# Optimization experiments

Hardware: AMD Instinct MI355X
Metric: run time of the kernel (lower is better)

The kernel has to match this reference:

```python
import jax, jax.numpy as jnp
import numpy as np

B, C, D, H, W = 8, 1, 128, 160, 128

def setup_inputs() -> dict:
    key = jax.random.key(0)
    kx, kb = jax.random.split(key)
    x = jax.random.normal(kx, (B, C, D, H, W), dtype=jnp.float32)
    base_volume = jax.random.normal(kb, (C, D, H, W), dtype=jnp.float32)
    return {"x": x, "base_volume": base_volume}

def reference(x, base_volume):
    # skimage match_histograms for continuous float images reduces (for a.e.-unique
    # values) to: map each source voxel's empirical CDF quantile onto the template's
    # inverse CDF via linear interpolation.
    tmpl = base_volume.ravel()
    t_sorted = jnp.sort(tmpl)                      # template inverse-CDF values
    M = tmpl.shape[0]
    tq = jnp.arange(1, M + 1, dtype=x.dtype) / M   # template CDF quantiles

    def match_one(sample):
        flat = sample.ravel()
        N = flat.shape[0]
        # rank of each voxel within its own sample (double argsort)
        ranks = jnp.argsort(jnp.argsort(flat))
        q = (ranks + 1).astype(flat.dtype) / N     # source empirical CDF
        matched = jnp.interp(q, tq, t_sorted)
        return matched.reshape(sample.shape)

    matched_vol = jax.vmap(match_one)(x)
    # self.model is identity here (the kernel headroom is the matching itself)
    return matched_vol
```

## Files before the change

kernel.cpp:

```cpp
#include <hip/hip_runtime.h>
#include <stdint.h>


#define SEG_N 2621440
#define NSEG 9
#define TILE 4096
#define NBLK (SEG_N / TILE)
#define RADIX 256
#define HL (RADIX * NBLK)
#define SCHUNK 4096
#define SNB (HL / SCHUNK)
#define SBUF (TILE + (TILE >> 4))

__device__ __forceinline__ uint32_t fkey(float f) {
  uint32_t b = __float_as_uint(f);
  return b ^ ((b & 0x80000000u) ? 0xFFFFFFFFu : 0x80000000u);
}
__device__ __forceinline__ float finv(uint32_t u) {
  uint32_t b = u ^ ((u & 0x80000000u) ? 0x80000000u : 0xFFFFFFFFu);
  return __uint_as_float(b);
}
__device__ __forceinline__ uint32_t SIDX(uint32_t i) { return i + (i >> 4); }

__global__ __launch_bounds__(256) void hist0_k(const float* __restrict__ x,
                                               const float* __restrict__ tmpl,
                                               int segbase,
                                               uint32_t* __restrict__ Hbk) {
  __shared__ uint32_t hw[4 * RADIX];
  const int t = threadIdx.x;
  const int blk = blockIdx.x;
  const int sl = blockIdx.y;
  const int seg = segbase + sl;
  const float* src = (seg == 0) ? tmpl : (x + (size_t)(seg - 1) * SEG_N);
  hw[t] = 0; hw[t + 256] = 0; hw[t + 512] = 0; hw[t + 768] = 0;
  __syncthreads();
  const int w = t >> 6;
  const float4* s4 = reinterpret_cast<const float4*>(src + blk * TILE);
#pragma unroll
  for (int r = 0; r < 4; ++r) {
    float4 v = s4[r * 256 + t];
    float f[4] = {v.x, v.y, v.z, v.w};
#pragma unroll
    for (int c = 0; c < 4; ++c)
      atomicAdd(&hw[w * 256 + (fkey(f[c]) & 255u)], 1u);
  }
  __syncthreads();
  Hbk[(size_t)sl * HL + (size_t)t * NBLK + blk] =
      hw[t] + hw[t + 256] + hw[t + 512] + hw[t + 768];
}

__global__ __launch_bounds__(256) void hist_k(const uint64_t* __restrict__ pairs,
                                              uint32_t* __restrict__ Hbk, int p) {
  __shared__ uint32_t hw[4 * RADIX];
  const int t = threadIdx.x;
  const int blk = blockIdx.x;
  const int sl = blockIdx.y;
  hw[t] = 0; hw[t + 256] = 0; hw[t + 512] = 0; hw[t + 768] = 0;
  __syncthreads();
  const int w = t >> 6;
  const int sh = 32 + 8 * p;
  const ulonglong2* pc = reinterpret_cast<const ulonglong2*>(
      pairs + (size_t)sl * SEG_N + (size_t)blk * TILE);
#pragma unroll
  for (int r = 0; r < 8; ++r) {
    ulonglong2 v = pc[r * 256 + t];
    atomicAdd(&hw[w * 256 + ((uint32_t)(v.x >> sh) & 255u)], 1u);
    atomicAdd(&hw[w * 256 + ((uint32_t)(v.y >> sh) & 255u)], 1u);
  }
  __syncthreads();
  Hbk[(size_t)sl * HL + (size_t)t * NBLK + blk] =
      hw[t] + hw[t + 256] + hw[t + 512] + hw[t + 768];
}

__global__ __launch_bounds__(256) void scanT_k(uint32_t* __restrict__ Hbk,
                                               uint32_t* __restrict__ desc) {
  __shared__ uint32_t lds[256];
  __shared__ uint32_t baseS;
  const int t = threadIdx.x;
  const int c = blockIdx.x;
  const int sl = blockIdx.y;
  uint32_t* base = Hbk + (size_t)sl * HL + (size_t)c * SCHUNK + (size_t)t * 16;
  uint4* p4 = reinterpret_cast<uint4*>(base);
  uint4 a[4];
  uint32_t s = 0;
#pragma unroll
  for (int k = 0; k < 4; ++k) {
    a[k] = p4[k];
    s += a[k].x + a[k].y + a[k].z + a[k].w;
  }
  lds[t] = s;
  __syncthreads();
#pragma unroll
  for (int off = 1; off < 256; off <<= 1) {
    uint32_t v = (t >= off) ? lds[t - off] : 0u;
    __syncthreads();
    lds[t] += v;
    __syncthreads();
  }
  const uint32_t incl = lds[t];
  const uint32_t total = lds[255];
  const uint32_t ex = incl - s;

  uint32_t* dseg = desc + sl * SNB;
  if (t == 0) {
    __hip_atomic_store(&dseg[c], (total & 0x3FFFFFFFu) |
                                     ((c == 0 ? 2u : 1u) << 30),
                       __ATOMIC_RELAXED, __HIP_MEMORY_SCOPE_AGENT);
    uint32_t acc = 0;
    if (c > 0) {
      int b = c - 1;
      bool done = false;
      while (!done) {
        uint32_t dv[8];
        const int n = (b >= 7) ? 8 : (b + 1);
#pragma unroll
        for (int i = 0; i < 8; ++i)
          if (i < n)
            dv[i] = __hip_atomic_load(&dseg[b - i], __ATOMIC_RELAXED,
                                      __HIP_MEMORY_SCOPE_AGENT);
        for (int i = 0; i < n; ++i) {
          uint32_t v = dv[i];
          while ((v >> 30) == 0u)
            v = __hip_atomic_load(&dseg[b - i], __ATOMIC_RELAXED,
                                  __HIP_MEMORY_SCOPE_AGENT);
          acc += v & 0x3FFFFFFFu;
          if ((v >> 30) == 2u) { done = true; break; }
        }
        b -= n;
        if (!done && b < 0) break;
      }
      __hip_atomic_store(&dseg[c], ((acc + total) & 0x3FFFFFFFu) | (2u << 30),
                         __ATOMIC_RELAXED, __HIP_MEMORY_SCOPE_AGENT);
    }
    baseS = acc;
  }
  __syncthreads();
  uint32_t run = baseS + ex;
#pragma unroll
  for (int k = 0; k < 4; ++k) {
    uint4 o;
    o.x = run; run += a[k].x;
    o.y = run; run += a[k].y;
    o.z = run; run += a[k].z;
    o.w = run; run += a[k].w;
    p4[k] = o;
  }
}

__device__ __forceinline__ void scan_pack2(uint32_t v0, uint32_t v1, uint32_t* s,
                                           uint32_t& ex0, uint32_t& ex1,
                                           uint32_t& tot0, uint32_t& tot1) {
  const int lane = threadIdx.x & 63, w = threadIdx.x >> 6;
  uint32_t a = v0, b = v1;
#pragma unroll
  for (int o = 1; o < 64; o <<= 1) {
    uint32_t na = __shfl_up(a, (unsigned)o, 64);
    uint32_t nb = __shfl_up(b, (unsigned)o, 64);
    if (lane >= o) { a += na; b += nb; }
  }
  if (lane == 63) { s[w] = a; s[4 + w] = b; }
  __syncthreads();
  if (threadIdx.x == 0) {
    uint32_t r0 = 0, r1 = 0;
#pragma unroll
    for (int i = 0; i < 4; ++i) {
      uint32_t q0 = s[i], q1 = s[4 + i];
      s[i] = r0; s[4 + i] = r1;
      r0 += q0; r1 += q1;
    }
    s[8] = r0; s[9] = r1;
  }
  __syncthreads();
  ex0 = a - v0 + s[w];
  ex1 = b - v1 + s[4 + w];
  tot0 = s[8]; tot1 = s[9];
  __syncthreads();
}

template <int P, int MODE>
__global__ __launch_bounds__(256) void part_k(const uint64_t* __restrict__ src,
                                              uint64_t* __restrict__ dst,
                                              const uint32_t* __restrict__ Hbk,
                                              const float* __restrict__ xin,
                                              const float* __restrict__ tmplin,
                                              float* __restrict__ tsorted,
                                              float* __restrict__ out,
                                              int segbase, int slbase) {
  __shared__ uint64_t buf[SBUF];
  __shared__ uint32_t ldsStart[RADIX];
  __shared__ uint32_t ldsBase[RADIX];
  __shared__ uint32_t scanS[12];
  const int t = threadIdx.x;
  const int blk = blockIdx.x;
  const int sl = slbase + blockIdx.y;
  const int seg = segbase + sl;

  ldsBase[t] = Hbk[(size_t)sl * HL + (size_t)t * NBLK + blk];

  if (MODE == 3) {
    const float* fsrc =
        (seg == 0) ? tmplin : (xin + (size_t)(seg - 1) * SEG_N);
    const float4* s4 = reinterpret_cast<const float4*>(fsrc + blk * TILE);
    const uint32_t base = (uint32_t)blk * TILE;
#pragma unroll
    for (int r = 0; r < 4; ++r) {
      float4 v = s4[r * 256 + t];
      uint32_t i0 = base + (uint32_t)(r * 256 + t) * 4u;
      float f[4] = {v.x, v.y, v.z, v.w};
#pragma unroll
      for (int c = 0; c < 4; ++c) {
        uint32_t k = fkey(f[c]);
        buf[SIDX((uint32_t)(r * 256 + t) * 4u + (uint32_t)c)] =
            ((uint64_t)k << 32) | (uint64_t)(i0 + c);
      }
    }
  } else {
    const uint64_t* ps = src + (size_t)sl * SEG_N + (size_t)blk * TILE;
#pragma unroll
    for (int r = 0; r < 16; ++r) buf[SIDX(r * 256 + t)] = ps[r * 256 + t];
  }
  __syncthreads();

  uint64_t e[16];
#pragma unroll
  for (int rnd = 0; rnd < 4; ++rnd) {
#pragma unroll
    for (int j = 0; j < 16; ++j) e[j] = buf[SIDX(t * 16 + j)];
    uint32_t cnt[4] = {0u, 0u, 0u, 0u};
#pragma unroll
    for (int j = 0; j < 16; ++j) {
      uint32_t d2 = (uint32_t)(e[j] >> (32 + 8 * P + 2 * rnd)) & 3u;
      cnt[d2]++;
    }
    uint32_t p0 = cnt[0] | (cnt[1] << 16);
    uint32_t p1 = cnt[2] | (cnt[3] << 16);
    uint32_t ex0, ex1, tot0, tot1;
    scan_pack2(p0, p1, scanS, ex0, ex1, tot0, tot1);
    uint32_t t0 = tot0 & 0xffffu, t1 = tot0 >> 16, t2 = tot1 & 0xffffu;
    uint32_t pos[4];
    pos[0] = (ex0 & 0xffffu);
    pos[1] = t0 + (ex0 >> 16);
    pos[2] = t0 + t1 + (ex1 & 0xffffu);
    pos[3] = t0 + t1 + t2 + (ex1 >> 16);
#pragma unroll
    for (int j = 0; j < 16; ++j) {
      uint32_t d2 = (uint32_t)(e[j] >> (32 + 8 * P + 2 * rnd)) & 3u;
      buf[SIDX(pos[d2]++)] = e[j];
    }
    __syncthreads();
  }

  const uint8_t* b8 = reinterpret_cast<const uint8_t*>(buf);
#pragma unroll
  for (int r = 0; r < 16; ++r) {
    uint32_t s = (uint32_t)(r * 256 + t);
    e[r] = buf[SIDX(s)];
    uint32_t d = (uint32_t)(e[r] >> (32 + 8 * P)) & 255u;
    uint32_t dp = (s == 0) ? 0x100u
                           : (uint32_t)b8[(size_t)SIDX(s - 1) * 8 + 4 + P];
    if (d != dp) ldsStart[d] = s;
  }
  __syncthreads();

#pragma unroll
  for (int r = 0; r < 16; ++r) {
    uint32_t s = (uint32_t)(r * 256 + t);
    uint64_t el = e[r];
    uint32_t key = (uint32_t)(el >> 32);
    uint32_t d = (key >> (8 * P)) & 255u;
    uint32_t dest = ldsBase[d] + s - ldsStart[d];
    if (MODE == 0 || MODE == 3) {
      dst[(size_t)sl * SEG_N + dest] = el;
    } else if (MODE == 1) {
      tsorted[dest] = finv(key);
    } else {
      out[(size_t)(seg - 1) * SEG_N + (uint32_t)el] = tsorted[dest];
    }
  }
}

extern "C" void kernel_launch(void* const* d_in, const int* in_sizes, int n_in,
                              void* d_out, int out_size, void* d_ws, size_t ws_size,
                              hipStream_t stream) {
  const float* x = (const float*)d_in[0];
  const float* tmpl = (const float*)d_in[1];
  float* out = (float*)d_out;

  auto need = [](int nb) -> size_t {
    return (size_t)nb * ((size_t)SEG_N * 16 + (size_t)HL * 4 + 4096) +
           (size_t)SEG_N * 4 + 16384;
  };
  const int nb = (ws_size >= need(9)) ? 9 : (ws_size >= need(3)) ? 3 : 1;

  uint8_t* w = (uint8_t*)d_ws;
  size_t off = 0;
  auto carve = [&](size_t bytes) -> void* {
    void* p = w + off;
    off = (off + bytes + 255) & ~(size_t)255;
    return p;
  };
  uint64_t* pairsA = (uint64_t*)carve((size_t)nb * SEG_N * 8);
  uint64_t* pairsB = (uint64_t*)carve((size_t)nb * SEG_N * 8);
  uint32_t* Hbk = (uint32_t*)carve((size_t)nb * HL * 4);
  uint32_t* desc = (uint32_t*)carve((size_t)4 * nb * SNB * 4);
  float* tsorted = (float*)carve((size_t)SEG_N * 4);

  for (int g = 0; g < NSEG; g += nb) {
    const dim3 gi(NBLK, nb);
    const dim3 gs(SNB, nb);

    hipMemsetAsync(desc, 0, (size_t)4 * nb * SNB * 4, stream);

    hist0_k<<<gi, 256, 0, stream>>>(x, tmpl, g, Hbk);
    scanT_k<<<gs, 256, 0, stream>>>(Hbk, desc + 0 * nb * SNB);
    part_k<0, 3><<<gi, 256, 0, stream>>>(nullptr, pairsA, Hbk, x, tmpl,
                                         tsorted, out, g, 0);
    hist_k<<<gi, 256, 0, stream>>>(pairsA, Hbk, 1);
    scanT_k<<<gs, 256, 0, stream>>>(Hbk, desc + 1 * nb * SNB);
    part_k<1, 0><<<gi, 256, 0, stream>>>(pairsA, pairsB, Hbk, nullptr, nullptr,
                                         tsorted, out, g, 0);
    hist_k<<<gi, 256, 0, stream>>>(pairsB, Hbk, 2);
    scanT_k<<<gs, 256, 0, stream>>>(Hbk, desc + 2 * nb * SNB);
    part_k<2, 0><<<gi, 256, 0, stream>>>(pairsB, pairsA, Hbk, nullptr, nullptr,
                                         tsorted, out, g, 0);
    hist_k<<<gi, 256, 0, stream>>>(pairsA, Hbk, 3);
    scanT_k<<<gs, 256, 0, stream>>>(Hbk, desc + 3 * nb * SNB);
    if (g == 0) {
      part_k<3, 1><<<dim3(NBLK, 1), 256, 0, stream>>>(
          pairsA, pairsB, Hbk, nullptr, nullptr, tsorted, out, g, 0);
      if (nb > 1)
        part_k<3, 2><<<dim3(NBLK, nb - 1), 256, 0, stream>>>(
            pairsA, pairsB, Hbk, nullptr, nullptr, tsorted, out, g, 1);
    } else {
      part_k<3, 2><<<dim3(NBLK, nb), 256, 0, stream>>>(
          pairsA, pairsB, Hbk, nullptr, nullptr, tsorted, out, g, 0);
    }
  }
}
```

Baseline: 1.104 ms.

## Fuse histogram prefix scan into histogram kernels via last-block-done pattern

Drops the separate scanT_k launches and their decoupled-lookback descriptor buffer. Each histogram block now bumps a per-segment atomic counter after writing its counts, and the last block to finish scans that segment's whole histogram table serially in chunks. This removes one kernel launch per radix pass and the descriptor memset. The cost is that the scan now runs on a single block per segment instead of many parallel blocks, which adds a serial tail at the end of each histogram kernel.

```diff
diff --git a/kernel.cpp b/kernel.cpp
--- a/kernel.cpp
+++ b/kernel.cpp
@@ -22,11 +22,80 @@
 }
 __device__ __forceinline__ uint32_t SIDX(uint32_t i) { return i + (i >> 4); }
 
+__device__ __forceinline__ void scan_segment(uint32_t* __restrict__ H,
+                                             uint32_t* __restrict__ sS) {
+  const int t = threadIdx.x;
+  const int lane = t & 63, w = t >> 6;
+  uint32_t carry = 0;
+  for (int c = 0; c < SNB; ++c) {
+    uint4* p4 = reinterpret_cast<uint4*>(H + (size_t)c * SCHUNK + (size_t)t * 16);
+    uint4 a[4];
+    uint32_t s = 0;
+#pragma unroll
+    for (int k = 0; k < 4; ++k) {
+      a[k] = p4[k];
+      s += a[k].x + a[k].y + a[k].z + a[k].w;
+    }
+    uint32_t is = s;
+#pragma unroll
+    for (int o = 1; o < 64; o <<= 1) {
+      uint32_t n = __shfl_up(is, (unsigned)o, 64);
+      if (lane >= o) is += n;
+    }
+    if (lane == 63) sS[w] = is;
+    __syncthreads();
+    if (t == 0) {
+      uint32_t r = 0;
+#pragma unroll
+      for (int i = 0; i < 4; ++i) { uint32_t q = sS[i]; sS[i] = r; r += q; }
+      sS[4] = r;
+    }
+    __syncthreads();
+    uint32_t run = carry + sS[w] + (is - s);
+    carry += sS[4];
+    __syncthreads();
+#pragma unroll
+    for (int k = 0; k < 4; ++k) {
+      uint4 o4;
+      o4.x = run; run += a[k].x;
+      o4.y = run; run += a[k].y;
+      o4.z = run; run += a[k].z;
+      o4.w = run; run += a[k].w;
+      p4[k] = o4;
+    }
+  }
+}
+
+__device__ __forceinline__ void hist_scan_epilogue(uint32_t* __restrict__ Hbk,
+                                                   uint32_t* __restrict__ cnt,
+                                                   int sl, uint32_t* __restrict__ sS) {
+  __shared__ uint32_t lastFlag;
+  const int t = threadIdx.x;
+  __syncthreads();
+  if (t == 0) {
+    __threadfence();
+    uint32_t old = __hip_atomic_fetch_add(&cnt[sl], 1u, __ATOMIC_ACQ_REL,
+                                          __HIP_MEMORY_SCOPE_AGENT);
+    lastFlag = (old == (uint32_t)NBLK - 1u);
+  }
+  __syncthreads();
+  if (lastFlag) {
+    __threadfence();
+    scan_segment(Hbk + (size_t)sl * HL, sS);
+    __syncthreads();
+    if (t == 0)
+      __hip_atomic_store(&cnt[sl], 0u, __ATOMIC_RELAXED,
+                         __HIP_MEMORY_SCOPE_AGENT);
+  }
+}
+
 __global__ __launch_bounds__(256) void hist0_k(const float* __restrict__ x,
                                                const float* __restrict__ tmpl,
                                                int segbase,
-                                               uint32_t* __restrict__ Hbk) {
+                                               uint32_t* __restrict__ Hbk,
+                                               uint32_t* __restrict__ cnt) {
   __shared__ uint32_t hw[4 * RADIX];
+  __shared__ uint32_t sS[8];
   const int t = threadIdx.x;
   const int blk = blockIdx.x;
   const int sl = blockIdx.y;
@@ -47,11 +116,14 @@
   __syncthreads();
   Hbk[(size_t)sl * HL + (size_t)t * NBLK + blk] =
       hw[t] + hw[t + 256] + hw[t + 512] + hw[t + 768];
+  hist_scan_epilogue(Hbk, cnt, sl, sS);
 }
 
 __global__ __launch_bounds__(256) void hist_k(const uint64_t* __restrict__ pairs,
-                                              uint32_t* __restrict__ Hbk, int p) {
+                                              uint32_t* __restrict__ Hbk, int p,
+                                              uint32_t* __restrict__ cnt) {
   __shared__ uint32_t hw[4 * RADIX];
+  __shared__ uint32_t sS[8];
   const int t = threadIdx.x;
   const int blk = blockIdx.x;
   const int sl = blockIdx.y;
@@ -70,81 +142,7 @@
   __syncthreads();
   Hbk[(size_t)sl * HL + (size_t)t * NBLK + blk] =
       hw[t] + hw[t + 256] + hw[t + 512] + hw[t + 768];
-}
-
-__global__ __launch_bounds__(256) void scanT_k(uint32_t* __restrict__ Hbk,
-                                               uint32_t* __restrict__ desc) {
-  __shared__ uint32_t lds[256];
-  __shared__ uint32_t baseS;
-  const int t = threadIdx.x;
-  const int c = blockIdx.x;
-  const int sl = blockIdx.y;
-  uint32_t* base = Hbk + (size_t)sl * HL + (size_t)c * SCHUNK + (size_t)t * 16;
-  uint4* p4 = reinterpret_cast<uint4*>(base);
-  uint4 a[4];
-  uint32_t s = 0;
-#pragma unroll
-  for (int k = 0; k < 4; ++k) {
-    a[k] = p4[k];
-    s += a[k].x + a[k].y + a[k].z + a[k].w;
-  }
-  lds[t] = s;
-  __syncthreads();
-#pragma unroll
-  for (int off = 1; off < 256; off <<= 1) {
-    uint32_t v = (t >= off) ? lds[t - off] : 0u;
-    __syncthreads();
-    lds[t] += v;
-    __syncthreads();
-  }
-  const uint32_t incl = lds[t];
-  const uint32_t total = lds[255];
-  const uint32_t ex = incl - s;
-
-  uint32_t* dseg = desc + sl * SNB;
-  if (t == 0) {
-    __hip_atomic_store(&dseg[c], (total & 0x3FFFFFFFu) |
-                                     ((c == 0 ? 2u : 1u) << 30),
-                       __ATOMIC_RELAXED, __HIP_MEMORY_SCOPE_AGENT);
-    uint32_t acc = 0;
-    if (c > 0) {
-      int b = c - 1;
-      bool done = false;
-      while (!done) {
-        uint32_t dv[8];
-        const int n = (b >= 7) ? 8 : (b + 1);
-#pragma unroll
-        for (int i = 0; i < 8; ++i)
-          if (i < n)
-            dv[i] = __hip_atomic_load(&dseg[b - i], __ATOMIC_RELAXED,
-                                      __HIP_MEMORY_SCOPE_AGENT);
-        for (int i = 0; i < n; ++i) {
-          uint32_t v = dv[i];
-          while ((v >> 30) == 0u)
-            v = __hip_atomic_load(&dseg[b - i], __ATOMIC_RELAXED,
-                                  __HIP_MEMORY_SCOPE_AGENT);
-          acc += v & 0x3FFFFFFFu;
-          if ((v >> 30) == 2u) { done = true; break; }
-        }
-        b -= n;
-        if (!done && b < 0) break;
-      }
-      __hip_atomic_store(&dseg[c], ((acc + total) & 0x3FFFFFFFu) | (2u << 30),
-                         __ATOMIC_RELAXED, __HIP_MEMORY_SCOPE_AGENT);
-    }
-    baseS = acc;
-  }
-  __syncthreads();
-  uint32_t run = baseS + ex;
-#pragma unroll
-  for (int k = 0; k < 4; ++k) {
-    uint4 o;
-    o.x = run; run += a[k].x;
-    o.y = run; run += a[k].y;
-    o.z = run; run += a[k].z;
-    o.w = run; run += a[k].w;
-    p4[k] = o;
-  }
+  hist_scan_epilogue(Hbk, cnt, sl, sS);
 }
 
 __device__ __forceinline__ void scan_pack2(uint32_t v0, uint32_t v1, uint32_t* s,
@@ -302,29 +300,24 @@
   uint64_t* pairsA = (uint64_t*)carve((size_t)nb * SEG_N * 8);
   uint64_t* pairsB = (uint64_t*)carve((size_t)nb * SEG_N * 8);
   uint32_t* Hbk = (uint32_t*)carve((size_t)nb * HL * 4);
-  uint32_t* desc = (uint32_t*)carve((size_t)4 * nb * SNB * 4);
+  uint32_t* cnt = (uint32_t*)carve(256);
   float* tsorted = (float*)carve((size_t)SEG_N * 4);
 
   for (int g = 0; g < NSEG; g += nb) {
     const dim3 gi(NBLK, nb);
-    const dim3 gs(SNB, nb);
-
-    hipMemsetAsync(desc, 0, (size_t)4 * nb * SNB * 4, stream);
-
-    hist0_k<<<gi, 256, 0, stream>>>(x, tmpl, g, Hbk);
-    scanT_k<<<gs, 256, 0, stream>>>(Hbk, desc + 0 * nb * SNB);
+
+    hipMemsetAsync(cnt, 0, 256, stream);
+
+    hist0_k<<<gi, 256, 0, stream>>>(x, tmpl, g, Hbk, cnt);
     part_k<0, 3><<<gi, 256, 0, stream>>>(nullptr, pairsA, Hbk, x, tmpl,
                                          tsorted, out, g, 0);
-    hist_k<<<gi, 256, 0, stream>>>(pairsA, Hbk, 1);
-    scanT_k<<<gs, 256, 0, stream>>>(Hbk, desc + 1 * nb * SNB);
+    hist_k<<<gi, 256, 0, stream>>>(pairsA, Hbk, 1, cnt);
     part_k<1, 0><<<gi, 256, 0, stream>>>(pairsA, pairsB, Hbk, nullptr, nullptr,
                                          tsorted, out, g, 0);
-    hist_k<<<gi, 256, 0, stream>>>(pairsB, Hbk, 2);
-    scanT_k<<<gs, 256, 0, stream>>>(Hbk, desc + 2 * nb * SNB);
+    hist_k<<<gi, 256, 0, stream>>>(pairsB, Hbk, 2, cnt);
     part_k<2, 0><<<gi, 256, 0, stream>>>(pairsB, pairsA, Hbk, nullptr, nullptr,
                                          tsorted, out, g, 0);
-    hist_k<<<gi, 256, 0, stream>>>(pairsA, Hbk, 3);
-    scanT_k<<<gs, 256, 0, stream>>>(Hbk, desc + 3 * nb * SNB);
+    hist_k<<<gi, 256, 0, stream>>>(pairsA, Hbk, 3, cnt);
     if (g == 0) {
       part_k<3, 1><<<dim3(NBLK, 1), 256, 0, stream>>>(
           pairsA, pairsB, Hbk, nullptr, nullptr, tsorted, out, g, 0);
```

New measurement: 3.247 ms. 2.94x slower.
